# Performance work log

Hardware: AMD Instinct MI355X
Metric: run time of the kernel (lower is better)

## Reference

```python
import jax, jax.numpy as jnp
import numpy as np

EPS_BN = 1e-5

def conv1(W, x):
    # 1x1 conv1d, no bias: W (Cout,Cin), x (B,Cin,N)
    return jnp.einsum('oc,bcn->bon', W, x)

def bn(x, g, b):
    # training-mode BatchNorm1d over (batch, points) per channel
    m = jnp.mean(x, axis=(0, 2), keepdims=True)
    v = jnp.mean((x - m) ** 2, axis=(0, 2), keepdims=True)
    return g[None, :, None] * (x - m) / jnp.sqrt(v + EPS_BN) + b[None, :, None]

def three_interpolation(p_dense, p_sparse, f_sparse):
    # p_dense (B,N1,3), p_sparse (B,N2,3), f_sparse (B,C,N2) -> (B,C,N1)
    d2 = jnp.sum((p_dense[:, :, None, :] - p_sparse[:, None, :, :]) ** 2, axis=-1)  # (B,N1,N2)
    neg, idx = jax.lax.top_k(-d2, 3)  # 3 nearest neighbors, (B,N1,3)
    w = 1.0 / (jnp.maximum(-neg, 0.0) + 1e-8)  # inverse (squared) distance, as pointnet2 three_nn
    w = w / jnp.sum(w, axis=-1, keepdims=True)
    gathered = jax.vmap(lambda f, i: f[:, i])(f_sparse, idx)  # (B,C,N1,3)
    return jnp.einsum('bcnk,bnk->bcn', gathered, w)

def fp(p_dense, f_skip, p_sparse, f_sparse, W1, g1, b1, W2, g2, b2):
    # FeaturePropogation upsample branch: concat(skip, interp) -> [conv1d+BN] x decoder_layers (act_args=None)
    x = jnp.concatenate([f_skip, three_interpolation(p_dense, p_sparse, f_sparse)], axis=1)
    x = bn(conv1(W1, x), g1, b1)
    x = bn(conv1(W2, x), g2, b2)
    return x

def setup_inputs():
    key = jax.random.key(0)
    ks = iter(jax.random.split(key, 40))
    B, N = 4, 8192
    Ns = [N, N, 2048, 512, 128]      # point counts of p0..p4 (strides 4)
    Cs = [128, 256, 512, 1024]       # encoder_channel_list
    d = {}
    for i in range(5):
        d[f'p{i}'] = jax.random.normal(next(ks), (B, Ns[i], 3), jnp.float32)
    for i in range(4):
        d[f'f{i + 1}'] = jax.random.normal(next(ks), (B, Cs[i], Ns[i + 1]), jnp.float32)
    d['cls_label'] = jax.random.randint(next(ks), (B, 1), 0, 16)
    # class-label convs: 16 -> 64 (BN+GELU) -> C0
    d['Wc1'] = jax.random.normal(next(ks), (64, 16), jnp.float32) * 0.1
    d['gc'] = jax.random.uniform(next(ks), (64,), jnp.float32, 0.5, 1.5)
    d['bc'] = jax.random.normal(next(ks), (64,), jnp.float32) * 0.1
    d['Wc2'] = jax.random.normal(next(ks), (Cs[0], 64), jnp.float32) * 0.1
    # decoder stages, coarsest (s2) to finest (s0)
    ins = [Cs[2] + Cs[3], Cs[1] + Cs[2], Cs[0] + Cs[1]]
    outs = [Cs[2], Cs[1], Cs[0]]
    for tag, ci, co in zip(['s2', 's1', 's0'], ins, outs):
        d[f'W{tag}a'] = jax.random.normal(next(ks), (co, ci), jnp.float32) * 0.05
        d[f'g{tag}a'] = jax.random.uniform(next(ks), (co,), jnp.float32, 0.5, 1.5)
        d[f'b{tag}a'] = jax.random.normal(next(ks), (co,), jnp.float32) * 0.1
        d[f'W{tag}b'] = jax.random.normal(next(ks), (co, co), jnp.float32) * 0.05
        d[f'g{tag}b'] = jax.random.uniform(next(ks), (co,), jnp.float32, 0.5, 1.5)
        d[f'b{tag}b'] = jax.random.normal(next(ks), (co,), jnp.float32) * 0.1
    return d

def reference(p0, p1, p2, p3, p4, f1, f2, f3, f4, cls_label,
              Wc1, gc, bc, Wc2,
              Ws2a, gs2a, bs2a, Ws2b, gs2b, bs2b,
              Ws1a, gs1a, bs1a, Ws1b, gs1b, bs1b,
              Ws0a, gs0a, bs0a, Ws0b, gs0b, bs0b):
    B, N = p0.shape[0], p0.shape[1]
    # one-hot class embedding broadcast over points, mapped 16 -> 64 -> C0
    one_hot = jax.nn.one_hot(cls_label[:, 0], 16, dtype=f1.dtype)  # (B,16)
    cls_feat = jnp.broadcast_to(one_hot[:, :, None], (B, 16, N))
    cls_feat = conv1(Wc2, jax.nn.gelu(bn(conv1(Wc1, cls_feat), gc, bc), approximate=False))
    # decoder stages, coarse to fine
    f3n = fp(p3, f3, p4, f4, Ws2a, gs2a, bs2a, Ws2b, gs2b, bs2b)   # (B,512,512)
    f2n = fp(p2, f2, p3, f3n, Ws1a, gs1a, bs1a, Ws1b, gs1b, bs1b)  # (B,256,2048)
    f1n = fp(p1, f1 + cls_feat, p2, f2n, Ws0a, gs0a, bs0a, Ws0b, gs0b, bs0b)  # (B,128,8192)
    return f1n
```

## Files before the change

### kernel.cpp

```cpp
#include <hip/hip_runtime.h>
#include <math.h>

#define BN_EPS 1e-5f

typedef float f32x4 __attribute__((ext_vector_type(4)));
typedef short s16x8 __attribute__((ext_vector_type(8)));
typedef short s16x4 __attribute__((ext_vector_type(4)));

__device__ __forceinline__ unsigned short f2bf(float f) {
    unsigned u = __builtin_bit_cast(unsigned, f);
    u = u + 0x7FFFu + ((u >> 16) & 1u);
    return (unsigned short)(u >> 16);
}
__device__ __forceinline__ float bf2f(unsigned short s) {
    unsigned u = ((unsigned)s) << 16;
    return __builtin_bit_cast(float, u);
}

__device__ __forceinline__ void gload16(const void* g, void* l) {
    __builtin_amdgcn_global_load_lds((const __attribute__((address_space(1))) unsigned int*)g,
                                     (__attribute__((address_space(3))) unsigned int*)l,
                                     16, 0, 0);
}

__global__ __launch_bounds__(256) void tr_all(const float* __restrict__ f1,
                                              const float* __restrict__ f2,
                                              const float* __restrict__ f3,
                                              const float* __restrict__ f4,
                                              unsigned short* __restrict__ F1T,
                                              unsigned short* __restrict__ F2T,
                                              unsigned short* __restrict__ F3T,
                                              unsigned short* __restrict__ F4T,
                                              const int* __restrict__ lbl,
                                              const float* __restrict__ Wc1,
                                              const float* __restrict__ gc,
                                              const float* __restrict__ bc,
                                              const float* __restrict__ Wc2) {
    __shared__ float t[32][33];
    __shared__ float clsv[32];
    __shared__ float hsh[4][64];
    __shared__ float actsh[4][64];
    int bx = blockIdx.x, b = blockIdx.y;
    const float* in; unsigned short* out; int C, N, nx, seg; bool docls = false;
    if (bx < 128)      { in = f4; out = F4T; C = 1024; N = 128;  nx = 4;   seg = bx; }
    else if (bx < 384) { in = f3; out = F3T; C = 512;  N = 512;  nx = 16;  seg = bx - 128; }
    else if (bx < 896) { in = f2; out = F2T; C = 256;  N = 2048; nx = 64;  seg = bx - 384; }
    else               { in = f1; out = F1T; C = 128;  N = 8192; nx = 256; seg = bx - 896; docls = true; }
    int n0 = (seg % nx) * 32, c0 = (seg / nx) * 32;
    int tid = threadIdx.x;
    if (docls) {
        { int b2 = tid >> 6, c = tid & 63; hsh[b2][c] = Wc1[c * 16 + lbl[b2]]; }
        __syncthreads();
        if (tid < 64) {
            int c = tid;
            float m = 0.f;
            for (int b2 = 0; b2 < 4; b2++) m += hsh[b2][c];
            m *= 0.25f;
            float v = 0.f;
            for (int b2 = 0; b2 < 4; b2++) { float d = hsh[b2][c] - m; v += d * d; }
            v *= 0.25f;
            float sc = gc[c] * rsqrtf(v + BN_EPS);
            float sh = bc[c] - m * sc;
            for (int b2 = 0; b2 < 4; b2++) {
                float x = hsh[b2][c] * sc + sh;
                actsh[b2][c] = 0.5f * x * (1.f + erff(x * 0.70710678118654752f));
            }
        }
        __syncthreads();
        if (tid < 32) {
            float s = 0.f;
            for (int c = 0; c < 64; c++) s += Wc2[(size_t)(c0 + tid) * 64 + c] * actsh[b][c];
            clsv[tid] = s;
        }
        __syncthreads();
    }
    int i = tid & 31, jj = tid >> 5;
#pragma unroll
    for (int j = jj; j < 32; j += 8) {
        float v = in[((size_t)b * C + c0 + j) * N + n0 + i];
        if (docls) v += clsv[j];
        t[j][i] = v;
    }
    __syncthreads();
    int j2 = tid & 31, i2b = tid >> 5;
#pragma unroll
    for (int i2 = i2b; i2 < 32; i2 += 8)
        out[((size_t)b * N + n0 + i2) * C + c0 + j2] = f2bf(t[j2][i2]);
}

template<int N2, int CHUNK, int STRIDE>
__device__ __forceinline__ void knn_body(const float* __restrict__ pd,
                                         const float* __restrict__ ps,
                                         int N1, int grp, int b,
                                         int* __restrict__ idx, float* __restrict__ w,
                                         float* spx, float* spy, float* spz) {
    int tid = threadIdx.x;
    for (int g = tid; g < N2; g += 256) {
        int s = g / CHUNK, off = g % CHUNK;
        size_t base = ((size_t)b * N2 + g) * 3;
        spx[s * STRIDE + off] = ps[base];
        spy[s * STRIDE + off] = ps[base + 1];
        spz[s * STRIDE + off] = ps[base + 2];
    }
    __syncthreads();
    int sub = tid & 7;
    int n = grp * 32 + (tid >> 3);
    size_t pb = ((size_t)b * N1 + n) * 3;
    float px = pd[pb], py = pd[pb + 1], pz = pd[pb + 2];
    float dd0 = 3.4e38f, dd1 = 3.4e38f, dd2 = 3.4e38f;
    int ii0 = 0, ii1 = 0, ii2 = 0;
    const float* rx = spx + sub * STRIDE;
    const float* ry = spy + sub * STRIDE;
    const float* rz = spz + sub * STRIDE;
    int jbase = sub * CHUNK;
    for (int t = 0; t < CHUNK; t += 4) {
        f32x4 x4 = *(const f32x4*)(rx + t);
        f32x4 y4 = *(const f32x4*)(ry + t);
        f32x4 z4 = *(const f32x4*)(rz + t);
#pragma unroll
        for (int e = 0; e < 4; e++) {
            float dx = px - x4[e], dy = py - y4[e], dz = pz - z4[e];
            float d = dx * dx + dy * dy + dz * dz;
            int j = jbase + t + e;
            bool C0 = d < dd0, C1 = d < dd1, C2 = d < dd2;
            int ni2 = C1 ? ii1 : (C2 ? j : ii2);
            int ni1 = C0 ? ii0 : (C1 ? j : ii1);
            int ni0 = C0 ? j : ii0;
            dd2 = __builtin_amdgcn_fmed3f(d, dd1, dd2);
            dd1 = __builtin_amdgcn_fmed3f(d, dd0, dd1);
            dd0 = fminf(d, dd0);
            ii0 = ni0; ii1 = ni1; ii2 = ni2;
        }
    }
    unsigned long long k0 = ((unsigned long long)__builtin_bit_cast(unsigned, dd0) << 32) | (unsigned)ii0;
    unsigned long long k1 = ((unsigned long long)__builtin_bit_cast(unsigned, dd1) << 32) | (unsigned)ii1;
    unsigned long long k2 = ((unsigned long long)__builtin_bit_cast(unsigned, dd2) << 32) | (unsigned)ii2;
#pragma unroll
    for (int m = 1; m < 8; m <<= 1) {
        unsigned long long e0, e1, e2;
        { int lo = __shfl_xor((int)(unsigned)(k0 & 0xFFFFFFFFull), m), hi = __shfl_xor((int)(unsigned)(k0 >> 32), m);
          e0 = ((unsigned long long)(unsigned)hi << 32) | (unsigned)lo; }
        { int lo = __shfl_xor((int)(unsigned)(k1 & 0xFFFFFFFFull), m), hi = __shfl_xor((int)(unsigned)(k1 >> 32), m);
          e1 = ((unsigned long long)(unsigned)hi << 32) | (unsigned)lo; }
        { int lo = __shfl_xor((int)(unsigned)(k2 & 0xFFFFFFFFull), m), hi = __shfl_xor((int)(unsigned)(k2 >> 32), m);
          e2 = ((unsigned long long)(unsigned)hi << 32) | (unsigned)lo; }
        unsigned long long t0, t1;
        t0 = k0 > e0 ? k0 : e0; k0 = k0 < e0 ? k0 : e0; t1 = k1 > t0 ? k1 : t0; k1 = k1 < t0 ? k1 : t0; k2 = k2 < t1 ? k2 : t1;
        t0 = k0 > e1 ? k0 : e1; k0 = k0 < e1 ? k0 : e1; t1 = k1 > t0 ? k1 : t0; k1 = k1 < t0 ? k1 : t0; k2 = k2 < t1 ? k2 : t1;
        t0 = k0 > e2 ? k0 : e2; k0 = k0 < e2 ? k0 : e2; t1 = k1 > t0 ? k1 : t0; k1 = k1 < t0 ? k1 : t0; k2 = k2 < t1 ? k2 : t1;
    }
    if (sub == 0) {
        float f0 = __builtin_bit_cast(float, (unsigned)(k0 >> 32));
        float f1 = __builtin_bit_cast(float, (unsigned)(k1 >> 32));
        float f2 = __builtin_bit_cast(float, (unsigned)(k2 >> 32));
        float w0 = 1.f / (f0 + 1e-8f), w1 = 1.f / (f1 + 1e-8f), w2 = 1.f / (f2 + 1e-8f);
        float s = 1.f / (w0 + w1 + w2);
        size_t o = ((size_t)b * N1 + n) * 3;
        idx[o] = (int)(unsigned)(k0 & 0xFFFFFFFFull);
        idx[o + 1] = (int)(unsigned)(k1 & 0xFFFFFFFFull);
        idx[o + 2] = (int)(unsigned)(k2 & 0xFFFFFFFFull);
        w[o] = w0 * s; w[o + 1] = w1 * s; w[o + 2] = w2 * s;
    }
}

__global__ __launch_bounds__(256) void knn_all(const float* __restrict__ p1,
                                               const float* __restrict__ p2,
                                               const float* __restrict__ p3,
                                               const float* __restrict__ p4,
                                               int* __restrict__ idx0, float* __restrict__ w0,
                                               int* __restrict__ idx1, float* __restrict__ w1,
                                               int* __restrict__ idx2, float* __restrict__ w2) {
    __shared__ float spx[8 * 264], spy[8 * 264], spz[8 * 264];
    int bx = blockIdx.x, b = blockIdx.y;
    if (bx < 16)      knn_body<128, 16, 24>(p3, p4, 512, bx, b, idx2, w2, spx, spy, spz);
    else if (bx < 80) knn_body<512, 64, 72>(p2, p3, 2048, bx - 16, b, idx1, w1, spx, spy, spz);
    else              knn_body<2048, 256, 264>(p1, p2, 8192, bx - 80, b, idx0, w0, spx, spy, spz);
}

__global__ __launch_bounds__(256) void build_x(const unsigned short* __restrict__ skipT,
                                               const unsigned short* __restrict__ fsT,
                                               const int* __restrict__ idx,
                                               const float* __restrict__ w,
                                               unsigned short* __restrict__ x,
                                               int Cskip, int Ctot, int Csp, int N1, int N2) {
    int cq = Ctot >> 3;
    size_t gid = (size_t)blockIdx.x * 256 + threadIdx.x;
    if (gid >= (size_t)4 * N1 * cq) return;
    int c = (int)(gid % cq) * 8;
    int n = (int)((gid / cq) % N1);
    int b = (int)(gid / ((size_t)cq * N1));
    s16x8 o;
    if (c < Cskip) {
        o = *(const s16x8*)(skipT + ((size_t)b * N1 + n) * Cskip + c);
    } else {
        int c2 = c - Cskip;
        size_t ob = ((size_t)b * N1 + n) * 3;
        int i0 = idx[ob], i1 = idx[ob + 1], i2 = idx[ob + 2];
        float w0 = w[ob], w1 = w[ob + 1], w2 = w[ob + 2];
        s16x8 v0 = *(const s16x8*)(fsT + ((size_t)b * N2 + i0) * Csp + c2);
        s16x8 v1 = *(const s16x8*)(fsT + ((size_t)b * N2 + i1) * Csp + c2);
        s16x8 v2 = *(const s16x8*)(fsT + ((size_t)b * N2 + i2) * Csp + c2);
#pragma unroll
        for (int j = 0; j < 8; j++) {
            float v = w0 * bf2f((unsigned short)v0[j]) + w1 * bf2f((unsigned short)v1[j]) + w2 * bf2f((unsigned short)v2[j]);
            o[j] = (short)f2bf(v);
        }
    }
    *(s16x8*)(x + ((size_t)b * N1 + n) * Ctot + c) = o;
}

__global__ __launch_bounds__(256) void wprep(const float* __restrict__ W,
                                             const float* __restrict__ sc,
                                             const float* __restrict__ sh,
                                             unsigned short* __restrict__ Wb,
                                             float* __restrict__ bias,
                                             int K, int kStart) {
    int m = blockIdx.x;
    int tid = threadIdx.x;
    float bsum = 0.f;
    for (int k = tid; k < K; k += 256) {
        float wv = W[(size_t)m * K + k];
        float o = wv;
        if (sc && k >= kStart) {
            o = wv * sc[k - kStart];
            bsum += wv * sh[k - kStart];
        }
        Wb[(size_t)m * K + k] = f2bf(o);
    }
    __shared__ float ls[256];
    ls[tid] = bsum;
    __syncthreads();
    for (int o = 128; o > 0; o >>= 1) {
        if (tid < o) ls[tid] += ls[tid + o];
        __syncthreads();
    }
    if (tid == 0) bias[m] = ls[0];
}

__global__ __launch_bounds__(256) void gemm64(const unsigned short* __restrict__ XT,
                                              const unsigned short* __restrict__ Wb,
                                              const float* __restrict__ bias,
                                              unsigned short* __restrict__ OutT,
                                              float* __restrict__ ps,
                                              int BN, int K, int M) {
    __shared__ unsigned short As[2][64 * 32];
    __shared__ unsigned short Bs[2][64 * 32];
    __shared__ float sred[2][2][32][2];
    int tid = threadIdx.x;
    int lane = tid & 63, wid = tid >> 6;
    int wn = wid & 1, wm = wid >> 1;
    int bx = blockIdx.x, by = blockIdx.y;

    int srow = (wid << 4) + (lane >> 2);
    int skcol = (lane & 3) << 3;
    const unsigned short* gA = XT + (size_t)(bx * 64 + srow) * K + skcol;
    const unsigned short* gB = Wb + (size_t)(by * 64 + srow) * K + skcol;

    f32x4 acc[2][2];
#pragma unroll
    for (int i = 0; i < 2; i++)
#pragma unroll
        for (int j = 0; j < 2; j++) acc[i][j] = (f32x4)0.f;

    int nt = K >> 5;
    gload16(gA, &As[0][wid * 512]);
    gload16(gB, &Bs[0][wid * 512]);

    int r16 = lane & 15, q = lane >> 4;
    for (int t = 0; t < nt; t++) {
        int cur = t & 1;
        if (t + 1 < nt) {
            int k0 = (t + 1) << 5;
            gload16(gA + k0, &As[cur ^ 1][wid * 512]);
            gload16(gB + k0, &Bs[cur ^ 1][wid * 512]);
            asm volatile("s_waitcnt vmcnt(2)" ::: "memory");
        } else {
            asm volatile("s_waitcnt vmcnt(0)" ::: "memory");
        }
        __syncthreads();
        s16x8 afr[2], bfr[2];
        afr[0] = *(const s16x8*)&As[cur][(wn * 32 + r16) * 32 + q * 8];
        afr[1] = *(const s16x8*)&As[cur][(wn * 32 + 16 + r16) * 32 + q * 8];
        bfr[0] = *(const s16x8*)&Bs[cur][(wm * 32 + r16) * 32 + q * 8];
        bfr[1] = *(const s16x8*)&Bs[cur][(wm * 32 + 16 + r16) * 32 + q * 8];
        asm volatile("s_waitcnt lgkmcnt(0)" ::: "memory");
        __builtin_amdgcn_sched_barrier(0);
        __syncthreads();
#pragma unroll
        for (int i = 0; i < 2; i++)
#pragma unroll
            for (int j = 0; j < 2; j++)
                acc[i][j] = __builtin_amdgcn_mfma_f32_16x16x32_bf16(afr[i], bfr[j], acc[i][j], 0, 0, 0);
    }

    int mc0 = by * 64 + wm * 32 + r16;
    float bv[2] = { bias[mc0], bias[mc0 + 16] };
    unsigned short* Ob = OutT + (size_t)(bx * 64) * M + by * 64;
    float s[2] = {0.f, 0.f}, qq[2] = {0.f, 0.f};
#pragma unroll
    for (int i = 0; i < 2; i++) {
#pragma unroll
        for (int j = 0; j < 2; j++) {
            int mcol = wm * 32 + j * 16 + r16;
#pragma unroll
            for (int r = 0; r < 4; r++) {
                float v = acc[i][j][r] + bv[j];
                s[j] += v; qq[j] += v * v;
                int n = wn * 32 + i * 16 + q * 4 + r;
                Ob[(size_t)n * M + mcol] = f2bf(v);
            }
        }
    }
#pragma unroll
    for (int j = 0; j < 2; j++) {
        s[j] += __shfl_xor(s[j], 16); s[j] += __shfl_xor(s[j], 32);
        qq[j] += __shfl_xor(qq[j], 16); qq[j] += __shfl_xor(qq[j], 32);
    }
    if (lane < 16) {
#pragma unroll
        for (int j = 0; j < 2; j++) {
            sred[wn][wm][j * 16 + lane][0] = s[j];
            sred[wn][wm][j * 16 + lane][1] = qq[j];
        }
    }
    __syncthreads();
    if (tid < 64) {
        int wmm = tid >> 5, c = tid & 31;
        float ssum = sred[0][wmm][c][0] + sred[1][wmm][c][0];
        float qsum = sred[0][wmm][c][1] + sred[1][wmm][c][1];
        size_t blin = (size_t)by * gridDim.x + bx;
        ps[blin * 128 + tid * 2] = ssum;
        ps[blin * 128 + tid * 2 + 1] = qsum;
    }
}

__global__ __launch_bounds__(256) void bn_finalize(const float* __restrict__ ps,
                                                   const float* __restrict__ g,
                                                   const float* __restrict__ bb,
                                                   float* __restrict__ sc,
                                                   float* __restrict__ sh,
                                                   int gx, int Npts) {
    int m = blockIdx.x;
    int by = m >> 6, ch = m & 63;
    float s = 0.f, q = 0.f;
    for (int bxi = threadIdx.x; bxi < gx; bxi += 256) {
        size_t blin = (size_t)by * gx + bxi;
        s += ps[blin * 128 + ch * 2];
        q += ps[blin * 128 + ch * 2 + 1];
    }
    __shared__ float ls[256], lq[256];
    ls[threadIdx.x] = s; lq[threadIdx.x] = q;
    __syncthreads();
    for (int o = 128; o > 0; o >>= 1) {
        if (threadIdx.x < o) { ls[threadIdx.x] += ls[threadIdx.x + o]; lq[threadIdx.x] += lq[threadIdx.x + o]; }
        __syncthreads();
    }
    if (threadIdx.x == 0) {
        float inv = 1.f / (float)Npts;
        float mean = ls[0] * inv;
        float var = fmaxf(lq[0] * inv - mean * mean, 0.f);
        float scale = g[m] * rsqrtf(var + BN_EPS);
        sc[m] = scale;
        sh[m] = bb[m] - mean * scale;
    }
}

__global__ __launch_bounds__(256) void out_bn_tr(const unsigned short* __restrict__ in,
                                                 float* __restrict__ out,
                                                 const float* __restrict__ sc,
                                                 const float* __restrict__ sh,
                                                 int M, int N) {
    __shared__ float t[32][33];
    int b = blockIdx.z;
    int n0 = blockIdx.x * 32, m0 = blockIdx.y * 32;
    int j = threadIdx.x & 31, ii = threadIdx.x >> 5;
#pragma unroll
    for (int i = ii; i < 32; i += 8)
        t[i][j] = bf2f(in[((size_t)b * N + n0 + i) * M + m0 + j]);
    __syncthreads();
    int i2 = threadIdx.x & 31, j2b = threadIdx.x >> 5;
#pragma unroll
    for (int j2 = j2b; j2 < 32; j2 += 8)
        out[((size_t)b * M + m0 + j2) * N + n0 + i2] = t[i2][j2] * sc[m0 + j2] + sh[m0 + j2];
}

extern "C" void kernel_launch(void* const* d_in, const int* in_sizes, int n_in,
                              void* d_out, int out_size, void* d_ws, size_t ws_size,
                              hipStream_t stream) {
    const float* p1 = (const float*)d_in[1];
    const float* p2 = (const float*)d_in[2];
    const float* p3 = (const float*)d_in[3];
    const float* p4 = (const float*)d_in[4];
    const float* f1 = (const float*)d_in[5];
    const float* f2 = (const float*)d_in[6];
    const float* f3 = (const float*)d_in[7];
    const float* f4 = (const float*)d_in[8];
    const int* cls = (const int*)d_in[9];
    const float* Wc1 = (const float*)d_in[10];
    const float* gc  = (const float*)d_in[11];
    const float* bc  = (const float*)d_in[12];
    const float* Wc2 = (const float*)d_in[13];
    const float* Ws2a = (const float*)d_in[14];
    const float* gs2a = (const float*)d_in[15];
    const float* bs2a = (const float*)d_in[16];
    const float* Ws2b = (const float*)d_in[17];
    const float* gs2b = (const float*)d_in[18];
    const float* bs2b = (const float*)d_in[19];
    const float* Ws1a = (const float*)d_in[20];
    const float* gs1a = (const float*)d_in[21];
    const float* bs1a = (const float*)d_in[22];
    const float* Ws1b = (const float*)d_in[23];
    const float* gs1b = (const float*)d_in[24];
    const float* bs1b = (const float*)d_in[25];
    const float* Ws0a = (const float*)d_in[26];
    const float* gs0a = (const float*)d_in[27];
    const float* bs0a = (const float*)d_in[28];
    const float* Ws0b = (const float*)d_in[29];
    const float* gs0b = (const float*)d_in[30];
    const float* bs0b = (const float*)d_in[31];

    char* ws = (char*)d_ws;
    size_t off = 0;
    auto alloc = [&](size_t bytes) { char* p = ws + off; off += (bytes + 255) & ~(size_t)255; return p; };
    unsigned short* F4T = (unsigned short*)alloc((size_t)4 * 128 * 1024 * 2);
    unsigned short* F3T = (unsigned short*)alloc((size_t)4 * 512 * 512 * 2);
    unsigned short* F2T = (unsigned short*)alloc((size_t)4 * 2048 * 256 * 2);
    unsigned short* F1T = (unsigned short*)alloc((size_t)4 * 8192 * 128 * 2);
    unsigned short* XS  = (unsigned short*)alloc((size_t)4 * 8192 * 384 * 2);
    unsigned short* YA  = (unsigned short*)alloc((size_t)4 * 8192 * 128 * 2);
    unsigned short* FN2 = (unsigned short*)alloc((size_t)4 * 512 * 512 * 2);
    unsigned short* FN1 = (unsigned short*)alloc((size_t)4 * 2048 * 256 * 2);
    unsigned short* XO  = (unsigned short*)alloc((size_t)4 * 8192 * 128 * 2);
    unsigned short* WB2a = (unsigned short*)alloc((size_t)512 * 1536 * 2);
    unsigned short* WB2b = (unsigned short*)alloc((size_t)512 * 512 * 2);
    unsigned short* WB1a = (unsigned short*)alloc((size_t)256 * 768 * 2);
    unsigned short* WB1b = (unsigned short*)alloc((size_t)256 * 256 * 2);
    unsigned short* WB0a = (unsigned short*)alloc((size_t)128 * 384 * 2);
    unsigned short* WB0b = (unsigned short*)alloc((size_t)128 * 128 * 2);
    float* BI2a = (float*)alloc(512 * 4); float* BI2b = (float*)alloc(512 * 4);
    float* BI1a = (float*)alloc(256 * 4); float* BI1b = (float*)alloc(256 * 4);
    float* BI0a = (float*)alloc(128 * 4); float* BI0b = (float*)alloc(128 * 4);
    int*   IDX0 = (int*)alloc((size_t)4 * 8192 * 3 * 4);
    float* WGT0 = (float*)alloc((size_t)4 * 8192 * 3 * 4);
    int*   IDX1 = (int*)alloc((size_t)4 * 2048 * 3 * 4);
    float* WGT1 = (float*)alloc((size_t)4 * 2048 * 3 * 4);
    int*   IDX2 = (int*)alloc((size_t)4 * 512 * 3 * 4);
    float* WGT2 = (float*)alloc((size_t)4 * 512 * 3 * 4);
    float* PS = (float*)alloc((size_t)1024 * 128 * 4);
    float* SC2a = (float*)alloc(512 * 4); float* SH2a = (float*)alloc(512 * 4);
    float* SC2b = (float*)alloc(512 * 4); float* SH2b = (float*)alloc(512 * 4);
    float* SC1a = (float*)alloc(512 * 4); float* SH1a = (float*)alloc(512 * 4);
    float* SC1b = (float*)alloc(512 * 4); float* SH1b = (float*)alloc(512 * 4);
    float* SC0a = (float*)alloc(512 * 4); float* SH0a = (float*)alloc(512 * 4);
    float* SC0b = (float*)alloc(512 * 4); float* SH0b = (float*)alloc(512 * 4);
    float* OUT = (float*)d_out;

    tr_all<<<dim3(1920, 4), 256, 0, stream>>>(f1, f2, f3, f4, F1T, F2T, F3T, F4T, cls, Wc1, gc, bc, Wc2);
    knn_all<<<dim3(336, 4), 256, 0, stream>>>(p1, p2, p3, p4, IDX0, WGT0, IDX1, WGT1, IDX2, WGT2);

    wprep<<<512, 256, 0, stream>>>(Ws2a, nullptr, nullptr, WB2a, BI2a, 1536, 0);
    build_x<<<(int)(((size_t)4 * 512 * (1536 / 8) + 255) / 256), 256, 0, stream>>>(
        F3T, F4T, IDX2, WGT2, XS, 512, 1536, 1024, 512, 128);
    gemm64<<<dim3(32, 8), 256, 0, stream>>>(XS, WB2a, BI2a, YA, PS, 2048, 1536, 512);
    bn_finalize<<<512, 256, 0, stream>>>(PS, gs2a, bs2a, SC2a, SH2a, 32, 2048);
    wprep<<<512, 256, 0, stream>>>(Ws2b, SC2a, SH2a, WB2b, BI2b, 512, 0);
    gemm64<<<dim3(32, 8), 256, 0, stream>>>(YA, WB2b, BI2b, FN2, PS, 2048, 512, 512);
    bn_finalize<<<512, 256, 0, stream>>>(PS, gs2b, bs2b, SC2b, SH2b, 32, 2048);

    wprep<<<256, 256, 0, stream>>>(Ws1a, SC2b, SH2b, WB1a, BI1a, 768, 256);
    build_x<<<(int)(((size_t)4 * 2048 * (768 / 8) + 255) / 256), 256, 0, stream>>>(
        F2T, FN2, IDX1, WGT1, XS, 256, 768, 512, 2048, 512);
    gemm64<<<dim3(128, 4), 256, 0, stream>>>(XS, WB1a, BI1a, YA, PS, 8192, 768, 256);
    bn_finalize<<<256, 256, 0, stream>>>(PS, gs1a, bs1a, SC1a, SH1a, 128, 8192);
    wprep<<<256, 256, 0, stream>>>(Ws1b, SC1a, SH1a, WB1b, BI1b, 256, 0);
    gemm64<<<dim3(128, 4), 256, 0, stream>>>(YA, WB1b, BI1b, FN1, PS, 8192, 256, 256);
    bn_finalize<<<256, 256, 0, stream>>>(PS, gs1b, bs1b, SC1b, SH1b, 128, 8192);

    wprep<<<128, 256, 0, stream>>>(Ws0a, SC1b, SH1b, WB0a, BI0a, 384, 128);
    build_x<<<(int)(((size_t)4 * 8192 * (384 / 8) + 255) / 256), 256, 0, stream>>>(
        F1T, FN1, IDX0, WGT0, XS, 128, 384, 256, 8192, 2048);
    gemm64<<<dim3(512, 2), 256, 0, stream>>>(XS, WB0a, BI0a, YA, PS, 32768, 384, 128);
    bn_finalize<<<128, 256, 0, stream>>>(PS, gs0a, bs0a, SC0a, SH0a, 512, 32768);
    wprep<<<128, 256, 0, stream>>>(Ws0b, SC0a, SH0a, WB0b, BI0b, 128, 0);
    gemm64<<<dim3(512, 2), 256, 0, stream>>>(YA, WB0b, BI0b, XO, PS, 32768, 128, 128);
    bn_finalize<<<128, 256, 0, stream>>>(PS, gs0b, bs0b, SC0b, SH0b, 512, 32768);

    out_bn_tr<<<dim3(8192 / 32, 128 / 32, 4), 256, 0, stream>>>(XO, OUT, SC0b, SH0b, 128, 8192);
}
```

Before: 200.0 us.

## Split finest-level KNN across candidate slices with a separate merge kernel

The finest KNN level (8192 queries against 2048 candidates) is now split into four candidate slices of 512, each handled by its own block. Each block writes its partial top-3 as packed distance/index keys, and a new merge kernel reduces the twelve keys per query to the final indices and weights. This raises block count from 336 to 1104 per batch and shrinks shared memory per block, aiming to improve occupancy and parallelism on the long serial candidate loop. The cost is an extra kernel launch and a global round trip for the partial results.

Measured after the change: 201.1 us. Within noise of the previous version (+0.6%).

```diff
diff --git a/kernel.cpp b/kernel.cpp
--- a/kernel.cpp
+++ b/kernel.cpp
@@ -88,16 +88,18 @@
         out[((size_t)b * N + n0 + i2) * C + c0 + j2] = f2bf(t[j2][i2]);
 }
 
-template<int N2, int CHUNK, int STRIDE>
+template<int CAND, int CHUNK, int STRIDE, bool PART>
 __device__ __forceinline__ void knn_body(const float* __restrict__ pd,
                                          const float* __restrict__ ps,
-                                         int N1, int grp, int b,
+                                         int N1, int N2total, int grp, int slice, int b,
                                          int* __restrict__ idx, float* __restrict__ w,
+                                         unsigned long long* __restrict__ pk, int nslice,
                                          float* spx, float* spy, float* spz) {
     int tid = threadIdx.x;
-    for (int g = tid; g < N2; g += 256) {
+    int cbase = slice * CAND;
+    for (int g = tid; g < CAND; g += 256) {
         int s = g / CHUNK, off = g % CHUNK;
-        size_t base = ((size_t)b * N2 + g) * 3;
+        size_t base = ((size_t)b * N2total + cbase + g) * 3;
         spx[s * STRIDE + off] = ps[base];
         spy[s * STRIDE + off] = ps[base + 1];
         spz[s * STRIDE + off] = ps[base + 2];
@@ -112,7 +114,7 @@
     const float* rx = spx + sub * STRIDE;
     const float* ry = spy + sub * STRIDE;
     const float* rz = spz + sub * STRIDE;
-    int jbase = sub * CHUNK;
+    int jbase = cbase + sub * CHUNK;
     for (int t = 0; t < CHUNK; t += 4) {
         f32x4 x4 = *(const f32x4*)(rx + t);
         f32x4 y4 = *(const f32x4*)(ry + t);
@@ -150,31 +152,65 @@
         t0 = k0 > e2 ? k0 : e2; k0 = k0 < e2 ? k0 : e2; t1 = k1 > t0 ? k1 : t0; k1 = k1 < t0 ? k1 : t0; k2 = k2 < t1 ? k2 : t1;
     }
     if (sub == 0) {
-        float f0 = __builtin_bit_cast(float, (unsigned)(k0 >> 32));
-        float f1 = __builtin_bit_cast(float, (unsigned)(k1 >> 32));
-        float f2 = __builtin_bit_cast(float, (unsigned)(k2 >> 32));
-        float w0 = 1.f / (f0 + 1e-8f), w1 = 1.f / (f1 + 1e-8f), w2 = 1.f / (f2 + 1e-8f);
-        float s = 1.f / (w0 + w1 + w2);
-        size_t o = ((size_t)b * N1 + n) * 3;
-        idx[o] = (int)(unsigned)(k0 & 0xFFFFFFFFull);
-        idx[o + 1] = (int)(unsigned)(k1 & 0xFFFFFFFFull);
-        idx[o + 2] = (int)(unsigned)(k2 & 0xFFFFFFFFull);
-        w[o] = w0 * s; w[o + 1] = w1 * s; w[o + 2] = w2 * s;
-    }
-}
-
-__global__ __launch_bounds__(256) void knn_all(const float* __restrict__ p1,
-                                               const float* __restrict__ p2,
-                                               const float* __restrict__ p3,
-                                               const float* __restrict__ p4,
-                                               int* __restrict__ idx0, float* __restrict__ w0,
-                                               int* __restrict__ idx1, float* __restrict__ w1,
-                                               int* __restrict__ idx2, float* __restrict__ w2) {
-    __shared__ float spx[8 * 264], spy[8 * 264], spz[8 * 264];
+        if (PART) {
+            size_t o = ((size_t)(b * N1 + n) * nslice + slice) * 3;
+            pk[o] = k0; pk[o + 1] = k1; pk[o + 2] = k2;
+        } else {
+            float f0 = __builtin_bit_cast(float, (unsigned)(k0 >> 32));
+            float f1 = __builtin_bit_cast(float, (unsigned)(k1 >> 32));
+            float f2 = __builtin_bit_cast(float, (unsigned)(k2 >> 32));
+            float w0 = 1.f / (f0 + 1e-8f), w1 = 1.f / (f1 + 1e-8f), w2 = 1.f / (f2 + 1e-8f);
+            float s = 1.f / (w0 + w1 + w2);
+            size_t o = ((size_t)b * N1 + n) * 3;
+            idx[o] = (int)(unsigned)(k0 & 0xFFFFFFFFull);
+            idx[o + 1] = (int)(unsigned)(k1 & 0xFFFFFFFFull);
+            idx[o + 2] = (int)(unsigned)(k2 & 0xFFFFFFFFull);
+            w[o] = w0 * s; w[o + 1] = w1 * s; w[o + 2] = w2 * s;
+        }
+    }
+}
+
+__global__ __launch_bounds__(256) void knn_part(const float* __restrict__ p1,
+                                                const float* __restrict__ p2,
+                                                const float* __restrict__ p3,
+                                                const float* __restrict__ p4,
+                                                int* __restrict__ idx1, float* __restrict__ w1,
+                                                int* __restrict__ idx2, float* __restrict__ w2,
+                                                unsigned long long* __restrict__ pk0) {
+    __shared__ float spx[8 * 72], spy[8 * 72], spz[8 * 72];
     int bx = blockIdx.x, b = blockIdx.y;
-    if (bx < 16)      knn_body<128, 16, 24>(p3, p4, 512, bx, b, idx2, w2, spx, spy, spz);
-    else if (bx < 80) knn_body<512, 64, 72>(p2, p3, 2048, bx - 16, b, idx1, w1, spx, spy, spz);
-    else              knn_body<2048, 256, 264>(p1, p2, 8192, bx - 80, b, idx0, w0, spx, spy, spz);
+    if (bx < 16)      knn_body<128, 16, 24, false>(p3, p4, 512, 128, bx, 0, b, idx2, w2, nullptr, 1, spx, spy, spz);
+    else if (bx < 80) knn_body<512, 64, 72, false>(p2, p3, 2048, 512, bx - 16, 0, b, idx1, w1, nullptr, 1, spx, spy, spz);
+    else {
+        int u = bx - 80;
+        knn_body<512, 64, 72, true>(p1, p2, 8192, 2048, u >> 2, u & 3, b, nullptr, nullptr, pk0, 4, spx, spy, spz);
+    }
+}
+
+__global__ __launch_bounds__(256) void knn_merge(const unsigned long long* __restrict__ pk,
+                                                 int* __restrict__ idx, float* __restrict__ w,
+                                                 int NQ) {
+    int q = blockIdx.x * 256 + threadIdx.x;
+    if (q >= NQ) return;
+    const unsigned long long* p = pk + (size_t)q * 12;
+    unsigned long long k0 = ~0ull, k1 = ~0ull, k2 = ~0ull;
+#pragma unroll
+    for (int i = 0; i < 12; i++) {
+        unsigned long long c = p[i];
+        unsigned long long t0 = k0 > c ? k0 : c; k0 = k0 < c ? k0 : c;
+        unsigned long long t1 = k1 > t0 ? k1 : t0; k1 = k1 < t0 ? k1 : t0;
+        k2 = k2 < t1 ? k2 : t1;
+    }
+    float f0 = __builtin_bit_cast(float, (unsigned)(k0 >> 32));
+    float f1 = __builtin_bit_cast(float, (unsigned)(k1 >> 32));
+    float f2 = __builtin_bit_cast(float, (unsigned)(k2 >> 32));
+    float w0 = 1.f / (f0 + 1e-8f), w1 = 1.f / (f1 + 1e-8f), w2 = 1.f / (f2 + 1e-8f);
+    float s = 1.f / (w0 + w1 + w2);
+    size_t o = (size_t)q * 3;
+    idx[o] = (int)(unsigned)(k0 & 0xFFFFFFFFull);
+    idx[o + 1] = (int)(unsigned)(k1 & 0xFFFFFFFFull);
+    idx[o + 2] = (int)(unsigned)(k2 & 0xFFFFFFFFull);
+    w[o] = w0 * s; w[o + 1] = w1 * s; w[o + 2] = w2 * s;
 }
 
 __global__ __launch_bounds__(256) void build_x(const unsigned short* __restrict__ skipT,
@@ -446,6 +482,7 @@
     float* WGT1 = (float*)alloc((size_t)4 * 2048 * 3 * 4);
     int*   IDX2 = (int*)alloc((size_t)4 * 512 * 3 * 4);
     float* WGT2 = (float*)alloc((size_t)4 * 512 * 3 * 4);
+    unsigned long long* PK0 = (unsigned long long*)alloc((size_t)4 * 8192 * 4 * 3 * 8);
     float* PS = (float*)alloc((size_t)1024 * 128 * 4);
     float* SC2a = (float*)alloc(512 * 4); float* SH2a = (float*)alloc(512 * 4);
     float* SC2b = (float*)alloc(512 * 4); float* SH2b = (float*)alloc(512 * 4);
@@ -456,7 +493,8 @@
     float* OUT = (float*)d_out;
 
     tr_all<<<dim3(1920, 4), 256, 0, stream>>>(f1, f2, f3, f4, F1T, F2T, F3T, F4T, cls, Wc1, gc, bc, Wc2);
-    knn_all<<<dim3(336, 4), 256, 0, stream>>>(p1, p2, p3, p4, IDX0, WGT0, IDX1, WGT1, IDX2, WGT2);
+    knn_part<<<dim3(1104, 4), 256, 0, stream>>>(p1, p2, p3, p4, IDX1, WGT1, IDX2, WGT2, PK0);
+    knn_merge<<<(4 * 8192) / 256, 256, 0, stream>>>(PK0, IDX0, WGT0, 4 * 8192);
 
     wprep<<<512, 256, 0, stream>>>(Ws2a, nullptr, nullptr, WB2a, BI2a, 1536, 0);
     build_x<<<(int)(((size_t)4 * 512 * (1536 / 8) + 255) / 256), 256, 0, stream>>>(
```
